# Optimization experiments

Measured on AMD Instinct MI355X. Metric: run time of the kernel, lower is better.

The kernel has to match this reference:

```python
import jax, jax.numpy as jnp
import numpy as np

MARGIN = 0.2
EPS = 1e-6


def setup_inputs() -> dict:
    key = jax.random.key(0)
    k1, k2 = jax.random.split(key)
    B, C = 8192, 1024
    z_label = jax.random.randint(k1, (B,), 0, 256, dtype=jnp.int64 if jax.config.jax_enable_x64 else jnp.int32)
    z_idx = jnp.arange(B, dtype=z_label.dtype)
    z = jax.random.normal(k2, (B, C), dtype=jnp.float32)
    return {"z_label": z_label, "z_idx": z_idx, "z": z}


def reference(z_label, z_idx, z):
    B = z.shape[0]
    k = max(2, int(B * 0.01))  # static: labels overwritten if batch has a single unique label
    all_same = jnp.all(z_label == z_label[0])
    z_label = jnp.where(all_same & (jnp.arange(B) < k), -1, z_label)

    # Vectorized triplet mining (replaces per-sample Python loop):
    # positive: first j with same label, different sample idx; negative: first j with different label.
    label_eq = z_label[:, None] == z_label[None, :]            # [B, B]
    pos_mask = label_eq & (z_idx[:, None] != z_idx[None, :])   # [B, B]
    neg_mask = ~label_eq                                       # [B, B]
    pos_idx = jnp.argmax(pos_mask, axis=1)  # first True (torch.where(...)[0][0])
    neg_idx = jnp.argmax(neg_mask, axis=1)
    valid = pos_mask.any(axis=1) & neg_mask.any(axis=1)        # [B]

    # TripletMarginLoss (p=2, swap=False): d(x,y) = ||x - y + eps||_2
    a, p_emb, n_emb = z, z[pos_idx], z[neg_idx]
    d_ap = jnp.sqrt(jnp.sum((a - p_emb + EPS) ** 2, axis=1))
    d_an = jnp.sqrt(jnp.sum((a - n_emb + EPS) ** 2, axis=1))
    per = jnp.maximum(d_ap - d_an + MARGIN, 0.0)               # [B]

    n_valid = valid.sum()
    vf = valid.astype(per.dtype)
    loss = jnp.where(n_valid > 0,
                     jnp.sum(per * vf) / jnp.maximum(n_valid, 1).astype(per.dtype),
                     jnp.array(0.0, per.dtype))
    return loss
```

## Files before the change

kernel.cpp:

```cpp
#include <hip/hip_runtime.h>

#define MARGIN 0.2f
#define EPSC 1e-6f

__device__ inline void acc8(const float4& av, const float4& pv, const float4& nv,
                            float& sap, float& san) {
    float d;
    d = av.x - pv.x + EPSC; sap += d * d;
    d = av.y - pv.y + EPSC; sap += d * d;
    d = av.z - pv.z + EPSC; sap += d * d;
    d = av.w - pv.w + EPSC; sap += d * d;
    d = av.x - nv.x + EPSC; san += d * d;
    d = av.y - nv.y + EPSC; san += d * d;
    d = av.z - nv.z + EPSC; san += d * d;
    d = av.w - nv.w + EPSC; san += d * d;
}

__global__ __launch_bounds__(256) void dist_kernel(
    const float* __restrict__ z, const int* __restrict__ label,
    const int* __restrict__ zidx, int B, int C, float2* __restrict__ g_part)
{
    const int wave = threadIdx.x >> 6;
    const int lane = threadIdx.x & 63;
    const int i = blockIdx.x * 4 + wave;

    float lsum = 0.f, lcnt = 0.f;
    if (i < B) {
        const int li    = label[i];
        const int myidx = zidx[i];

        const float4* a = (const float4*)(z + (size_t)i * C) + lane;
        float4 a0, a1, a2, a3;
        const bool c1024 = (C == 1024);
        if (c1024) { a0 = a[0]; a1 = a[64]; a2 = a[128]; a3 = a[192]; }

        int pos = -1, neg = -1;
        for (int j0 = 0; j0 < B && (pos < 0 || neg < 0); j0 += 64) {
            const int j = j0 + lane;
            const bool inb = j < B;
            int lj = 0, xj = 0;
            if (inb) { lj = label[j]; xj = zidx[j]; }
            unsigned long long pb = __ballot(inb && lj == li && xj != myidx);
            unsigned long long nb = __ballot(inb && lj != li);
            if (pos < 0 && pb) pos = j0 + (__ffsll((unsigned long long)pb) - 1);
            if (neg < 0 && nb) neg = j0 + (__ffsll((unsigned long long)nb) - 1);
        }
        if (neg < 0) {
            int k = B / 100; if (k < 2) k = 2;
            const int l0  = li;
            const int lie = (i < k) ? -1 : l0;
            pos = -1; neg = -1;
            for (int j0 = 0; j0 < B && (pos < 0 || neg < 0); j0 += 64) {
                const int j = j0 + lane;
                const bool inb = j < B;
                int xj = 0;
                if (inb) xj = zidx[j];
                const int lje = (j < k) ? -1 : l0;
                unsigned long long pb = __ballot(inb && lje == lie && xj != myidx);
                unsigned long long nb = __ballot(inb && lje != lie);
                if (pos < 0 && pb) pos = j0 + (__ffsll((unsigned long long)pb) - 1);
                if (neg < 0 && nb) neg = j0 + (__ffsll((unsigned long long)nb) - 1);
            }
        }
        const bool valid = (pos >= 0) && (neg >= 0);
        const int pi = pos < 0 ? 0 : pos;
        const int ni = neg < 0 ? 0 : neg;

        const float4* p = (const float4*)(z + (size_t)pi * C) + lane;
        const float4* n = (const float4*)(z + (size_t)ni * C) + lane;
        float sap = 0.f, san = 0.f;
        if (c1024) {
            float4 p0 = p[0], p1 = p[64], p2 = p[128], p3 = p[192];
            float4 n0 = n[0], n1 = n[64], n2 = n[128], n3 = n[192];
            acc8(a0, p0, n0, sap, san);
            acc8(a1, p1, n1, sap, san);
            acc8(a2, p2, n2, sap, san);
            acc8(a3, p3, n3, sap, san);
        } else {
            const int nk = C >> 8;
            for (int kk = 0; kk < nk; ++kk)
                acc8(a[kk * 64], p[kk * 64], n[kk * 64], sap, san);
            for (int c = (nk << 8) + lane; c < C; c += 64) {
                float av = z[(size_t)i * C + c];
                float pv = z[(size_t)pi * C + c];
                float nv = z[(size_t)ni * C + c];
                float d = av - pv + EPSC; sap += d * d;
                d = av - nv + EPSC; san += d * d;
            }
        }
        for (int off = 32; off; off >>= 1) {
            sap += __shfl_xor(sap, off, 64);
            san += __shfl_xor(san, off, 64);
        }
        if (lane == 0 && valid) {
            lsum = fmaxf(sqrtf(sap) - sqrtf(san) + MARGIN, 0.f);
            lcnt = 1.f;
        }
    }

    __shared__ float s_sum[4], s_cnt[4];
    if (lane == 0) { s_sum[wave] = lsum; s_cnt[wave] = lcnt; }
    __syncthreads();
    if (threadIdx.x == 0) {
        float bs = 0.f, bc = 0.f;
        for (int w = 0; w < 4; ++w) { bs += s_sum[w]; bc += s_cnt[w]; }
        g_part[blockIdx.x] = make_float2(bs, bc);
    }
}

__global__ __launch_bounds__(1024) void final_kernel(
    const float2* __restrict__ g_part, int nb, float* __restrict__ out)
{
    const int t = threadIdx.x;
    float s = 0.f, c = 0.f;
    for (int idx = t; idx < nb; idx += blockDim.x) {
        float2 v = g_part[idx];
        s += v.x; c += v.y;
    }
    for (int off = 32; off; off >>= 1) {
        s += __shfl_xor(s, off, 64);
        c += __shfl_xor(c, off, 64);
    }
    __shared__ float s_s[16], s_c[16];
    const int wave = t >> 6, lane = t & 63;
    if (lane == 0) { s_s[wave] = s; s_c[wave] = c; }
    __syncthreads();
    if (t == 0) {
        float ts = 0.f, tc = 0.f;
        const int nw = blockDim.x >> 6;
        for (int w = 0; w < nw; ++w) { ts += s_s[w]; tc += s_c[w]; }
        out[0] = (tc > 0.f) ? ts / tc : 0.f;
    }
}

extern "C" void kernel_launch(void* const* d_in, const int* in_sizes, int n_in,
                              void* d_out, int out_size, void* d_ws, size_t ws_size,
                              hipStream_t stream) {
    const int*   z_label = (const int*)d_in[0];
    const int*   z_idx   = (const int*)d_in[1];
    const float* z       = (const float*)d_in[2];
    const int B = in_sizes[0];
    const int C = in_sizes[2] / B;
    float* out = (float*)d_out;

    const int nblk = (B + 3) / 4;
    float2* g_part = (float2*)d_ws;

    dist_kernel<<<nblk, 256, 0, stream>>>(z, z_label, z_idx, B, C, g_part);
    final_kernel<<<1, 1024, 0, stream>>>(g_part, nblk, out);
}
```

Measured before the change: 89.35 us.

## Process two anchor rows per wave with int4-vectorized label scan

Each wave now handles two anchor rows, sharing one label/index scan between them, and the scan reads four labels per lane as int4 so each step covers 256 candidates. The all-same-label fallback is replaced by a closed-form search that sets the negative directly and only scans for the positive. This cuts the number of scan iterations and label loads, and halves the block count. In exchange each wave holds more registers and does more serial work, which may lower occupancy and latency hiding.

Result: faster. 85.09 us (-4.8%).

```diff
diff --git a/kernel.cpp b/kernel.cpp
--- a/kernel.cpp
+++ b/kernel.cpp
@@ -16,72 +16,127 @@
     d = av.w - nv.w + EPSC; san += d * d;
 }
 
+__device__ inline void scan4(const int4& lj, const int4& xj, int li, int myidx,
+                             int j0, int& pos, int& neg) {
+    if (pos < 0) {
+        int m = ((lj.x == li && xj.x != myidx) ? 1 : 0)
+              | ((lj.y == li && xj.y != myidx) ? 2 : 0)
+              | ((lj.z == li && xj.z != myidx) ? 4 : 0)
+              | ((lj.w == li && xj.w != myidx) ? 8 : 0);
+        unsigned long long b = __ballot(m != 0);
+        if (b) {
+            int L  = __ffsll(b) - 1;
+            int mL = __shfl(m, L, 64);
+            pos = j0 + L * 4 + (__ffs(mL) - 1);
+        }
+    }
+    if (neg < 0) {
+        int m = ((lj.x != li) ? 1 : 0) | ((lj.y != li) ? 2 : 0)
+              | ((lj.z != li) ? 4 : 0) | ((lj.w != li) ? 8 : 0);
+        unsigned long long b = __ballot(m != 0);
+        if (b) {
+            int L  = __ffsll(b) - 1;
+            int mL = __shfl(m, L, 64);
+            neg = j0 + L * 4 + (__ffs(mL) - 1);
+        }
+    }
+}
+
+__device__ inline void mine_row_64(const int* __restrict__ label,
+                                   const int* __restrict__ zidx, int B, int lane,
+                                   int li, int myidx, int& pos, int& neg) {
+    pos = -1; neg = -1;
+    for (int j0 = 0; j0 < B && (pos < 0 || neg < 0); j0 += 64) {
+        int j = j0 + lane;
+        bool inb = j < B;
+        int lj = 0, xj = 0;
+        if (inb) { lj = label[j]; xj = zidx[j]; }
+        unsigned long long pb = __ballot(inb && lj == li && xj != myidx);
+        unsigned long long nb = __ballot(inb && lj != li);
+        if (pos < 0 && pb) pos = j0 + __ffsll(pb) - 1;
+        if (neg < 0 && nb) neg = j0 + __ffsll(nb) - 1;
+    }
+}
+
+__device__ inline void mine_allsame(const int* __restrict__ zidx, int B, int lane,
+                                    int i, int myidx, int& pos, int& neg) {
+    int k = B / 100; if (k < 2) k = 2;
+    int kk = k < B ? k : B;
+    int lo, hi;
+    if (i < kk) { lo = 0;  hi = kk; neg = (kk < B) ? kk : -1; }
+    else        { lo = kk; hi = B;  neg = 0; }
+    pos = -1;
+    for (int j0 = lo; j0 < hi && pos < 0; j0 += 64) {
+        int j = j0 + lane;
+        bool ok = (j < hi) && (zidx[j] != myidx);
+        unsigned long long b = __ballot(ok);
+        if (b) pos = j0 + __ffsll(b) - 1;
+    }
+}
+
 __global__ __launch_bounds__(256) void dist_kernel(
     const float* __restrict__ z, const int* __restrict__ label,
     const int* __restrict__ zidx, int B, int C, float2* __restrict__ g_part)
 {
     const int wave = threadIdx.x >> 6;
     const int lane = threadIdx.x & 63;
-    const int i = blockIdx.x * 4 + wave;
+    const int ia = blockIdx.x * 8 + wave * 2;
+    const int ib = ia + 1;
+    const bool hasA = ia < B, hasB = ib < B;
+    const bool c1024 = (C == 1024);
 
     float lsum = 0.f, lcnt = 0.f;
-    if (i < B) {
-        const int li    = label[i];
-        const int myidx = zidx[i];
-
-        const float4* a = (const float4*)(z + (size_t)i * C) + lane;
-        float4 a0, a1, a2, a3;
-        const bool c1024 = (C == 1024);
-        if (c1024) { a0 = a[0]; a1 = a[64]; a2 = a[128]; a3 = a[192]; }
-
-        int pos = -1, neg = -1;
-        for (int j0 = 0; j0 < B && (pos < 0 || neg < 0); j0 += 64) {
-            const int j = j0 + lane;
-            const bool inb = j < B;
-            int lj = 0, xj = 0;
-            if (inb) { lj = label[j]; xj = zidx[j]; }
-            unsigned long long pb = __ballot(inb && lj == li && xj != myidx);
-            unsigned long long nb = __ballot(inb && lj != li);
-            if (pos < 0 && pb) pos = j0 + (__ffsll((unsigned long long)pb) - 1);
-            if (neg < 0 && nb) neg = j0 + (__ffsll((unsigned long long)nb) - 1);
-        }
-        if (neg < 0) {
-            int k = B / 100; if (k < 2) k = 2;
-            const int l0  = li;
-            const int lie = (i < k) ? -1 : l0;
-            pos = -1; neg = -1;
-            for (int j0 = 0; j0 < B && (pos < 0 || neg < 0); j0 += 64) {
-                const int j = j0 + lane;
-                const bool inb = j < B;
-                int xj = 0;
-                if (inb) xj = zidx[j];
-                const int lje = (j < k) ? -1 : l0;
-                unsigned long long pb = __ballot(inb && lje == lie && xj != myidx);
-                unsigned long long nb = __ballot(inb && lje != lie);
-                if (pos < 0 && pb) pos = j0 + (__ffsll((unsigned long long)pb) - 1);
-                if (neg < 0 && nb) neg = j0 + (__ffsll((unsigned long long)nb) - 1);
+
+    int liA = 0, idxA = 0, liB = 0, idxB = 0;
+    if (hasA) { liA = label[ia]; idxA = zidx[ia]; }
+    if (hasB) { liB = label[ib]; idxB = zidx[ib]; }
+
+    const float4* aA = (const float4*)(z + (size_t)ia * C) + lane;
+    const float4* aB = (const float4*)(z + (size_t)ib * C) + lane;
+    float4 A0, A1, A2, A3, Bb0, Bb1, Bb2, Bb3;
+    if (hasA && c1024) { A0 = aA[0]; A1 = aA[64]; A2 = aA[128]; A3 = aA[192]; }
+    if (hasB && c1024) { Bb0 = aB[0]; Bb1 = aB[64]; Bb2 = aB[128]; Bb3 = aB[192]; }
+
+    int posA = -1, negA = -1, posB = -1, negB = -1;
+    if (hasA) {
+        if ((B & 255) == 0) {
+            if (!hasB) { posB = 0; negB = 0; }
+            for (int j0 = 0; j0 < B && (posA < 0 || negA < 0 || posB < 0 || negB < 0);
+                 j0 += 256) {
+                const int base = j0 + lane * 4;
+                int4 lj = *(const int4*)(label + base);
+                int4 xj = *(const int4*)(zidx + base);
+                scan4(lj, xj, liA, idxA, j0, posA, negA);
+                if (hasB) scan4(lj, xj, liB, idxB, j0, posB, negB);
             }
-        }
-        const bool valid = (pos >= 0) && (neg >= 0);
-        const int pi = pos < 0 ? 0 : pos;
-        const int ni = neg < 0 ? 0 : neg;
-
+        } else {
+            mine_row_64(label, zidx, B, lane, liA, idxA, posA, negA);
+            if (hasB) mine_row_64(label, zidx, B, lane, liB, idxB, posB, negB);
+        }
+        if (negA < 0) {
+            mine_allsame(zidx, B, lane, ia, idxA, posA, negA);
+            if (hasB) mine_allsame(zidx, B, lane, ib, idxB, posB, negB);
+        }
+    }
+
+    if (hasA) {
+        const int pi = posA < 0 ? 0 : posA;
+        const int ni = negA < 0 ? 0 : negA;
         const float4* p = (const float4*)(z + (size_t)pi * C) + lane;
         const float4* n = (const float4*)(z + (size_t)ni * C) + lane;
         float sap = 0.f, san = 0.f;
         if (c1024) {
             float4 p0 = p[0], p1 = p[64], p2 = p[128], p3 = p[192];
             float4 n0 = n[0], n1 = n[64], n2 = n[128], n3 = n[192];
-            acc8(a0, p0, n0, sap, san);
-            acc8(a1, p1, n1, sap, san);
-            acc8(a2, p2, n2, sap, san);
-            acc8(a3, p3, n3, sap, san);
+            acc8(A0, p0, n0, sap, san); acc8(A1, p1, n1, sap, san);
+            acc8(A2, p2, n2, sap, san); acc8(A3, p3, n3, sap, san);
         } else {
+            const float4* a = (const float4*)(z + (size_t)ia * C) + lane;
             const int nk = C >> 8;
             for (int kk = 0; kk < nk; ++kk)
                 acc8(a[kk * 64], p[kk * 64], n[kk * 64], sap, san);
             for (int c = (nk << 8) + lane; c < C; c += 64) {
-                float av = z[(size_t)i * C + c];
+                float av = z[(size_t)ia * C + c];
                 float pv = z[(size_t)pi * C + c];
                 float nv = z[(size_t)ni * C + c];
                 float d = av - pv + EPSC; sap += d * d;
@@ -92,9 +147,43 @@
             sap += __shfl_xor(sap, off, 64);
             san += __shfl_xor(san, off, 64);
         }
-        if (lane == 0 && valid) {
-            lsum = fmaxf(sqrtf(sap) - sqrtf(san) + MARGIN, 0.f);
-            lcnt = 1.f;
+        if (lane == 0 && posA >= 0 && negA >= 0) {
+            lsum += fmaxf(sqrtf(sap) - sqrtf(san) + MARGIN, 0.f);
+            lcnt += 1.f;
+        }
+    }
+
+    if (hasB) {
+        const int pi = posB < 0 ? 0 : posB;
+        const int ni = negB < 0 ? 0 : negB;
+        const float4* p = (const float4*)(z + (size_t)pi * C) + lane;
+        const float4* n = (const float4*)(z + (size_t)ni * C) + lane;
+        float sap = 0.f, san = 0.f;
+        if (c1024) {
+            float4 p0 = p[0], p1 = p[64], p2 = p[128], p3 = p[192];
+            float4 n0 = n[0], n1 = n[64], n2 = n[128], n3 = n[192];
+            acc8(Bb0, p0, n0, sap, san); acc8(Bb1, p1, n1, sap, san);
+            acc8(Bb2, p2, n2, sap, san); acc8(Bb3, p3, n3, sap, san);
+        } else {
+            const float4* a = (const float4*)(z + (size_t)ib * C) + lane;
+            const int nk = C >> 8;
+            for (int kk = 0; kk < nk; ++kk)
+                acc8(a[kk * 64], p[kk * 64], n[kk * 64], sap, san);
+            for (int c = (nk << 8) + lane; c < C; c += 64) {
+                float av = z[(size_t)ib * C + c];
+                float pv = z[(size_t)pi * C + c];
+                float nv = z[(size_t)ni * C + c];
+                float d = av - pv + EPSC; sap += d * d;
+                d = av - nv + EPSC; san += d * d;
+            }
+        }
+        for (int off = 32; off; off >>= 1) {
+            sap += __shfl_xor(sap, off, 64);
+            san += __shfl_xor(san, off, 64);
+        }
+        if (lane == 0 && posB >= 0 && negB >= 0) {
+            lsum += fmaxf(sqrtf(sap) - sqrtf(san) + MARGIN, 0.f);
+            lcnt += 1.f;
         }
     }
 
@@ -143,7 +232,7 @@
     const int C = in_sizes[2] / B;
     float* out = (float*)d_out;
 
-    const int nblk = (B + 3) / 4;
+    const int nblk = (B + 7) / 8;
     float2* g_part = (float2*)d_ws;
 
     dist_kernel<<<nblk, 256, 0, stream>>>(z, z_label, z_idx, B, C, g_part);
```
